# Optimization experiments

Measured on AMD Instinct MI355X. Metric: run time of the kernel, lower is better.

The kernel has to match this reference:

```python
import jax, jax.numpy as jnp
import numpy as np

B, N_TOK, C = 16, 4096, 512
TIME_DIM = 512
H_HEADS, WS = 8, 8
HEAD_DIM = C // H_HEADS
RES = 64  # sqrt(N_TOK)
NH = NW = RES // WS
SCALE = HEAD_DIM ** -0.5


def _rel_pos_index(ws):
    coords = np.stack(np.meshgrid(np.arange(ws), np.arange(ws), indexing='ij'))  # (2,ws,ws)
    flat = coords.reshape(2, -1)  # (2, ws*ws)
    rel = flat[:, :, None] - flat[:, None, :]  # (2, N, N)
    rel = rel.transpose(1, 2, 0).astype(np.int64)
    rel[:, :, 0] += ws - 1
    rel[:, :, 1] += ws - 1
    rel[:, :, 0] *= 2 * ws - 1
    return rel.sum(-1)  # (ws*ws, ws*ws)

REL_IDX = jnp.asarray(_rel_pos_index(WS))


def setup_inputs() -> dict:
    key = jax.random.key(0)
    ks = jax.random.split(key, 9)
    return {
        'x': jax.random.normal(ks[0], (B, N_TOK, C), jnp.float32),
        'time_emb': jax.random.normal(ks[1], (B, TIME_DIM), jnp.float32),
        'Wqkv': jax.random.normal(ks[2], (3 * C, C), jnp.float32) * 0.02,
        'bqkv': jnp.zeros((3 * C,), jnp.float32),
        'Wt': jax.random.normal(ks[3], (3 * C, TIME_DIM), jnp.float32) * 0.02,
        'bt': jnp.zeros((3 * C,), jnp.float32),
        'Wo': jax.random.normal(ks[4], (C, C), jnp.float32) * 0.02,
        'bo': jnp.zeros((C,), jnp.float32),
        'bias_table': jax.random.normal(ks[5], ((2 * WS - 1) ** 2, H_HEADS), jnp.float32) * 0.02,
    }


def reference(x, time_emb, Wqkv, bqkv, Wt, bt, Wo, bo, bias_table):
    Bo = x.shape[0]
    # window partition: (B, H*W, C) -> (B*nH*nW, ws*ws, C)
    xw = x.reshape(Bo, NH, WS, NW, WS, C).transpose(0, 1, 3, 2, 4, 5).reshape(-1, WS * WS, C)
    Bw, N = xw.shape[0], WS * WS
    # time emb broadcast to every window: (Bw, time_dim)
    te = jnp.broadcast_to(time_emb[:, None, :], (Bo, NH * NW, TIME_DIM)).reshape(Bw, TIME_DIM)
    # spatial qkv: (Bw, N, 3, h, d) -> q/k/v (Bw, h, N, d)
    qkv_s = (xw @ Wqkv.T + bqkv).reshape(Bw, N, 3, H_HEADS, HEAD_DIM).transpose(2, 0, 3, 1, 4)
    # time qkv: (Bw, 3, h, d) -> (3, Bw, h, 1, d)
    qkv_t = (te @ Wt.T + bt).reshape(Bw, 1, 3, H_HEADS, HEAD_DIM).transpose(2, 0, 3, 1, 4)
    q = qkv_s[0] + qkv_t[0]
    k = qkv_s[1] + qkv_t[1]
    v = qkv_s[2] + qkv_t[2]
    # relative position bias: (h, N, N)
    bias = bias_table[REL_IDX.reshape(-1)].reshape(N, N, H_HEADS).transpose(2, 0, 1)
    attn = jnp.einsum('bhnd,bhmd->bhnm', q, k) * SCALE + bias[None]
    attn = jax.nn.softmax(attn, axis=-1)
    out = jnp.einsum('bhnm,bhmd->bhnd', attn, v)
    out = out.transpose(0, 2, 1, 3).reshape(Bw, N, C)
    out = out @ Wo.T + bo
    # NOTE: source module's unpartition condition (ws^2 < ws^2) is False -> stays windowed
    return out
```

## Files before the change

### kernel.cpp

```cpp
#include <hip/hip_runtime.h>

using u16 = unsigned short;
typedef __bf16 bf16x8 __attribute__((ext_vector_type(8)));
typedef float floatx4 __attribute__((ext_vector_type(4)));

__device__ __forceinline__ u16 f2bf(float f) {
    union { float f; unsigned u; } v; v.f = f;
    unsigned r = v.u + 0x7fffu + ((v.u >> 16) & 1u);
    return (u16)(r >> 16);
}

__device__ __forceinline__ void gld16(const void* g, void* l) {
    __builtin_amdgcn_global_load_lds(
        (const __attribute__((address_space(1))) void*)g,
        (__attribute__((address_space(3))) void*)l, 16, 0, 0);
}

__device__ __forceinline__ void cvt4(const float* __restrict__ src,
                                     u16* __restrict__ dst, int i) {
    float4 v = *(const float4*)(src + i);
    ushort4 o;
    o.x = f2bf(v.x); o.y = f2bf(v.y); o.z = f2bf(v.z); o.w = f2bf(v.w);
    *(ushort4*)(dst + i) = o;
}

__global__ __launch_bounds__(256) void prep_k(
    const float* __restrict__ x, const float* __restrict__ Wqkv,
    const float* __restrict__ Wo, const float* __restrict__ te,
    const float* __restrict__ Wt, const float* __restrict__ bt,
    const float* __restrict__ btab,
    u16* __restrict__ xbf, u16* __restrict__ wqkvbf, u16* __restrict__ wobf,
    float* __restrict__ qkvt, float* __restrict__ biasf)
{
    const int b = blockIdx.x, tid = threadIdx.x;
    if (b < 768) {
        cvt4(Wqkv, wqkvbf, b * 1024 + tid * 4);
    } else if (b < 1024) {
        cvt4(Wo, wobf, (b - 768) * 1024 + tid * 4);
    } else if (b < 1120) {
        const int bb = b - 1024;
        const int batch = bb / 6;
        const int c = (bb % 6) * 256 + tid;
        const float4* a4 = (const float4*)(te + batch * 512);
        const float4* w4 = (const float4*)(Wt + (size_t)c * 512);
        float s = 0.f;
        for (int i = 0; i < 128; ++i) {
            float4 av = a4[i], wv = w4[i];
            s += av.x * wv.x + av.y * wv.y + av.z * wv.z + av.w * wv.w;
        }
        qkvt[batch * 1536 + c] = s + bt[c];
    } else if (b < 1152) {
        const int e0 = (b - 1120) * 1024 + tid;
        for (int k = 0; k < 4; ++k) {
            int e = e0 + k * 256;
            int h = e >> 12, rc = e & 4095, row = rc >> 6, col = rc & 63;
            int idx = ((row >> 3) - (col >> 3) + 7) * 15 + ((row & 7) - (col & 7) + 7);
            biasf[e] = btab[idx * 8 + h];
        }
    } else {
        const int base = (b - 1152) * 4096 + tid * 4;
        for (int k = 0; k < 4; ++k) cvt4(x, xbf, base + k * 1024);
    }
}

__global__ __launch_bounds__(256, 3) void gemm_qkv_k(
    const u16* __restrict__ A, const u16* __restrict__ B,
    const float* __restrict__ bqkv, const float* __restrict__ qkvt,
    u16* __restrict__ C)
{
    __shared__ __align__(16) u16 lA[128 * 32];
    __shared__ __align__(16) u16 lB[128 * 32];
    const int tid = threadIdx.x;
    const int lane = tid & 63, wv = tid >> 6;
    const int ln = lane & 15, quad = lane >> 4;

    const int orig = blockIdx.y * 12 + blockIdx.x;
    const int wgid = (orig & 7) * 768 + (orig >> 3);
    const int tm = wgid / 12, tn = wgid % 12;

    const int wm = (wv & 1) * 64, wn = (wv >> 1) * 64;

    floatx4 acc[4][4];
#pragma unroll
    for (int i = 0; i < 4; ++i)
#pragma unroll
        for (int j = 0; j < 4; ++j) acc[i][j] = (floatx4){0.f, 0.f, 0.f, 0.f};

    const int srow = tid >> 2, scb = tid & 3;
    const u16* ag = A + (size_t)(tm * 128 + srow) * 512 + scb * 8;
    const u16* bg = B + (size_t)(tn * 128 + srow) * 512 + scb * 8;
    u16* la0 = &lA[tid * 8];
    u16* la1 = &lA[2048 + tid * 8];
    u16* lb0 = &lB[tid * 8];
    u16* lb1 = &lB[2048 + tid * 8];

    for (int k0 = 0; k0 < 512; k0 += 32) {
        __syncthreads();
        gld16(ag + k0, la0);
        gld16(ag + 64 * 512 + k0, la1);
        gld16(bg + k0, lb0);
        gld16(bg + 64 * 512 + k0, lb1);
        __syncthreads();
        bf16x8 af[4], bf[4];
#pragma unroll
        for (int mt = 0; mt < 4; ++mt)
            af[mt] = *(const bf16x8*)&lA[(wm + mt * 16 + ln) * 32 + quad * 8];
#pragma unroll
        for (int nt = 0; nt < 4; ++nt)
            bf[nt] = *(const bf16x8*)&lB[(wn + nt * 16 + ln) * 32 + quad * 8];
#pragma unroll
        for (int mt = 0; mt < 4; ++mt)
#pragma unroll
            for (int nt = 0; nt < 4; ++nt)
                acc[mt][nt] = __builtin_amdgcn_mfma_f32_16x16x32_bf16(
                    af[mt], bf[nt], acc[mt][nt], 0, 0, 0);
    }

    const float* qt = qkvt + (tm >> 5) * 1536;
#pragma unroll
    for (int nt = 0; nt < 4; ++nt) {
        const int col = tn * 128 + wn + nt * 16 + ln;
        const float add = bqkv[col] + qt[col];
#pragma unroll
        for (int mt = 0; mt < 4; ++mt) {
            const int row0 = tm * 128 + wm + mt * 16 + quad * 4;
#pragma unroll
            for (int r = 0; r < 4; ++r)
                C[(size_t)(row0 + r) * 1536 + col] = f2bf(acc[mt][nt][r] + add);
        }
    }
}

__global__ __launch_bounds__(256, 4) void attn_k(
    const u16* __restrict__ qkv, const float* __restrict__ biasf,
    u16* __restrict__ aout)
{
    __shared__ __align__(16) u16 sbuf[4][64 * 72];
    const int tid = threadIdx.x, lane = tid & 63, wv = tid >> 6;
    const int ln = lane & 15, quad = lane >> 4;
    const int pair = blockIdx.x * 4 + wv;
    const int w = pair >> 3, h = pair & 7;
    const int bb = w >> 6, nh = (w >> 3) & 7, nw = w & 7;
    const int tbase = bb * 4096 + nh * 512 + nw * 8;
    u16* buf = sbuf[wv];

    {
        const int wj = lane >> 3;
        const int d0 = (lane & 7) * 8;
#pragma unroll
        for (int i = 0; i < 8; ++i) {
            const int t = tbase + i * 64 + wj;
            union { bf16x8 v; u16 u[8]; } cv;
            cv.v = *(const bf16x8*)(qkv + (size_t)t * 1536 + 1024 + h * 64 + d0);
            const int n = i * 8 + wj;
#pragma unroll
            for (int j = 0; j < 8; ++j) buf[(d0 + j) * 72 + n] = cv.u[j];
        }
    }

    bf16x8 vtf[4][2];
#pragma unroll
    for (int dt = 0; dt < 4; ++dt) {
        const u16* vr = &buf[(dt * 16 + ln) * 72 + quad * 8];
        vtf[dt][0] = *(const bf16x8*)vr;
        vtf[dt][1] = *(const bf16x8*)(vr + 32);
    }

    bf16x8 kf[4][2];
#pragma unroll
    for (int nt = 0; nt < 4; ++nt) {
        const int n = nt * 16 + ln;
        const int t = tbase + (n >> 3) * 64 + (n & 7);
        const u16* kr = qkv + (size_t)t * 1536 + 512 + h * 64 + quad * 8;
        kf[nt][0] = *(const bf16x8*)kr;
        kf[nt][1] = *(const bf16x8*)(kr + 32);
    }

#pragma unroll
    for (int mt = 0; mt < 4; ++mt) {
        const int m = mt * 16 + ln;
        const int t = tbase + (m >> 3) * 64 + (m & 7);
        const u16* qr = qkv + (size_t)t * 1536 + h * 64 + quad * 8;
        const bf16x8 qf0 = *(const bf16x8*)qr;
        const bf16x8 qf1 = *(const bf16x8*)(qr + 32);
        floatx4 s[4];
        __builtin_amdgcn_s_setprio(1);
#pragma unroll
        for (int nt = 0; nt < 4; ++nt) {
            s[nt] = (floatx4){0.f, 0.f, 0.f, 0.f};
            s[nt] = __builtin_amdgcn_mfma_f32_16x16x32_bf16(qf0, kf[nt][0], s[nt], 0, 0, 0);
            s[nt] = __builtin_amdgcn_mfma_f32_16x16x32_bf16(qf1, kf[nt][1], s[nt], 0, 0, 0);
        }
        __builtin_amdgcn_s_setprio(0);
        float z[4][4];
        const float* bptr = biasf + h * 4096 + (mt * 16 + quad * 4) * 64 + ln;
#pragma unroll
        for (int nt = 0; nt < 4; ++nt)
#pragma unroll
            for (int r = 0; r < 4; ++r)
                z[nt][r] = s[nt][r] * 0.125f + bptr[r * 64 + nt * 16];
        float pmax[4], prcp[4];
#pragma unroll
        for (int r = 0; r < 4; ++r) {
            float v = fmaxf(fmaxf(z[0][r], z[1][r]), fmaxf(z[2][r], z[3][r]));
            v = fmaxf(v, __shfl_xor(v, 1));
            v = fmaxf(v, __shfl_xor(v, 2));
            v = fmaxf(v, __shfl_xor(v, 4));
            v = fmaxf(v, __shfl_xor(v, 8));
            pmax[r] = v;
        }
#pragma unroll
        for (int nt = 0; nt < 4; ++nt)
#pragma unroll
            for (int r = 0; r < 4; ++r)
                z[nt][r] = __expf(z[nt][r] - pmax[r]);
#pragma unroll
        for (int r = 0; r < 4; ++r) {
            float v = z[0][r] + z[1][r] + z[2][r] + z[3][r];
            v += __shfl_xor(v, 1);
            v += __shfl_xor(v, 2);
            v += __shfl_xor(v, 4);
            v += __shfl_xor(v, 8);
            prcp[r] = __builtin_amdgcn_rcpf(v);
        }
#pragma unroll
        for (int nt = 0; nt < 4; ++nt)
#pragma unroll
            for (int r = 0; r < 4; ++r)
                buf[(mt * 16 + quad * 4 + r) * 72 + nt * 16 + ln] =
                    f2bf(z[nt][r] * prcp[r]);
    }

#pragma unroll
    for (int mt = 0; mt < 4; ++mt) {
        const u16* pr = &buf[(mt * 16 + ln) * 72 + quad * 8];
        const bf16x8 pf0 = *(const bf16x8*)pr;
        const bf16x8 pf1 = *(const bf16x8*)(pr + 32);
#pragma unroll
        for (int dt = 0; dt < 4; ++dt) {
            floatx4 o = (floatx4){0.f, 0.f, 0.f, 0.f};
            __builtin_amdgcn_s_setprio(1);
            o = __builtin_amdgcn_mfma_f32_16x16x32_bf16(pf0, vtf[dt][0], o, 0, 0, 0);
            o = __builtin_amdgcn_mfma_f32_16x16x32_bf16(pf1, vtf[dt][1], o, 0, 0, 0);
            __builtin_amdgcn_s_setprio(0);
            const size_t rbase =
                (size_t)(w * 64 + mt * 16 + quad * 4) * 512 + h * 64 + dt * 16 + ln;
#pragma unroll
            for (int r = 0; r < 4; ++r)
                aout[rbase + (size_t)r * 512] = f2bf(o[r]);
        }
    }
}

__global__ __launch_bounds__(256, 3) void gemm_out_k(
    const u16* __restrict__ A, const u16* __restrict__ B,
    const float* __restrict__ bo, float* __restrict__ C)
{
    __shared__ __align__(16) u16 lA[128 * 32];
    __shared__ __align__(16) u16 lB[128 * 32];
    const int tid = threadIdx.x;
    const int lane = tid & 63, wv = tid >> 6;
    const int ln = lane & 15, quad = lane >> 4;

    const int orig = blockIdx.y * 4 + blockIdx.x;
    const int wgid = (orig & 7) * 256 + (orig >> 3);
    const int tm = wgid >> 2, tn = wgid & 3;

    const int wm = (wv & 1) * 64, wn = (wv >> 1) * 64;

    floatx4 acc[4][4];
#pragma unroll
    for (int i = 0; i < 4; ++i)
#pragma unroll
        for (int j = 0; j < 4; ++j) acc[i][j] = (floatx4){0.f, 0.f, 0.f, 0.f};

    const int srow = tid >> 2, scb = tid & 3;
    const u16* ag = A + (size_t)(tm * 128 + srow) * 512 + scb * 8;
    const u16* bg = B + (size_t)(tn * 128 + srow) * 512 + scb * 8;
    u16* la0 = &lA[tid * 8];
    u16* la1 = &lA[2048 + tid * 8];
    u16* lb0 = &lB[tid * 8];
    u16* lb1 = &lB[2048 + tid * 8];

    for (int k0 = 0; k0 < 512; k0 += 32) {
        __syncthreads();
        gld16(ag + k0, la0);
        gld16(ag + 64 * 512 + k0, la1);
        gld16(bg + k0, lb0);
        gld16(bg + 64 * 512 + k0, lb1);
        __syncthreads();
        bf16x8 af[4], bf[4];
#pragma unroll
        for (int mt = 0; mt < 4; ++mt)
            af[mt] = *(const bf16x8*)&lA[(wm + mt * 16 + ln) * 32 + quad * 8];
#pragma unroll
        for (int nt = 0; nt < 4; ++nt)
            bf[nt] = *(const bf16x8*)&lB[(wn + nt * 16 + ln) * 32 + quad * 8];
#pragma unroll
        for (int mt = 0; mt < 4; ++mt)
#pragma unroll
            for (int nt = 0; nt < 4; ++nt)
                acc[mt][nt] = __builtin_amdgcn_mfma_f32_16x16x32_bf16(
                    af[mt], bf[nt], acc[mt][nt], 0, 0, 0);
    }

#pragma unroll
    for (int nt = 0; nt < 4; ++nt) {
        const int col = tn * 128 + wn + nt * 16 + ln;
        const float add = bo[col];
#pragma unroll
        for (int mt = 0; mt < 4; ++mt) {
            const int row0 = tm * 128 + wm + mt * 16 + quad * 4;
#pragma unroll
            for (int r = 0; r < 4; ++r)
                C[(size_t)(row0 + r) * 512 + col] = acc[mt][nt][r] + add;
        }
    }
}

extern "C" void kernel_launch(void* const* d_in, const int* in_sizes, int n_in,
                              void* d_out, int out_size, void* d_ws, size_t ws_size,
                              hipStream_t stream)
{
    const float* x    = (const float*)d_in[0];
    const float* te   = (const float*)d_in[1];
    const float* Wqkv = (const float*)d_in[2];
    const float* bqkv = (const float*)d_in[3];
    const float* Wt   = (const float*)d_in[4];
    const float* bt   = (const float*)d_in[5];
    const float* Wo   = (const float*)d_in[6];
    const float* bo   = (const float*)d_in[7];
    const float* btab = (const float*)d_in[8];
    float* out = (float*)d_out;

    char* w = (char*)d_ws;
    u16*   xbf    = (u16*)(w);
    u16*   qkvbf  = (u16*)(w + 67108864);
    u16*   wqkvbf = (u16*)(w + 268435456);
    u16*   wobf   = (u16*)(w + 270008320);
    float* qkvt   = (float*)(w + 270532608);
    float* biasf  = (float*)(w + 270630912);

    prep_k<<<9344, 256, 0, stream>>>(x, Wqkv, Wo, te, Wt, bt, btab,
                                     xbf, wqkvbf, wobf, qkvt, biasf);
    gemm_qkv_k<<<dim3(12, 512), 256, 0, stream>>>(xbf, wqkvbf, bqkv, qkvt, qkvbf);
    attn_k<<<2048, 256, 0, stream>>>(qkvbf, biasf, xbf );
    gemm_out_k<<<dim3(4, 512), 256, 0, stream>>>(xbf, wobf, bo, out);
}
```

Before: 507.1 us.

## Fuse four kernels into one persistent cooperative kernel with grid syncs

```diff
diff --git a/kernel.cpp b/kernel.cpp
--- a/kernel.cpp
+++ b/kernel.cpp
@@ -1,4 +1,7 @@
 #include <hip/hip_runtime.h>
+#include <hip/hip_cooperative_groups.h>
+
+namespace cg = cooperative_groups;
 
 using u16 = unsigned short;
 typedef __bf16 bf16x8 __attribute__((ext_vector_type(8)));
@@ -22,6 +25,311 @@
     ushort4 o;
     o.x = f2bf(v.x); o.y = f2bf(v.y); o.z = f2bf(v.z); o.w = f2bf(v.w);
     *(ushort4*)(dst + i) = o;
+}
+
+__global__ __launch_bounds__(256, 3) void mega_k(
+    const float* __restrict__ x, const float* __restrict__ te,
+    const float* __restrict__ Wqkv, const float* __restrict__ bqkv,
+    const float* __restrict__ Wt, const float* __restrict__ bt,
+    const float* __restrict__ Wo, const float* __restrict__ bo,
+    const float* __restrict__ btab, float* __restrict__ out,
+    char* __restrict__ ws)
+{
+    u16*   xbf    = (u16*)(ws);
+    u16*   qkvbf  = (u16*)(ws + 67108864);
+    u16*   wqkvbf = (u16*)(ws + 268435456);
+    u16*   wobf   = (u16*)(ws + 270008320);
+    float* qkvt   = (float*)(ws + 270532608);
+    float* biasf  = (float*)(ws + 270630912);
+
+    __shared__ __align__(16) u16 smem[18432];
+    u16* lA = smem;
+    u16* lB = smem + 4096;
+
+    cg::grid_group grid = cg::this_grid();
+    const int tid = threadIdx.x;
+    const int lane = tid & 63, wv = tid >> 6;
+    const int ln = lane & 15, quad = lane >> 4;
+    const int nb = gridDim.x;
+
+    for (int b = blockIdx.x; b < 9344; b += nb) {
+        if (b < 768) {
+            cvt4(Wqkv, wqkvbf, b * 1024 + tid * 4);
+        } else if (b < 1024) {
+            cvt4(Wo, wobf, (b - 768) * 1024 + tid * 4);
+        } else if (b < 1120) {
+            const int bb = b - 1024;
+            const int batch = bb / 6;
+            const int c = (bb % 6) * 256 + tid;
+            const float4* a4 = (const float4*)(te + batch * 512);
+            const float4* w4 = (const float4*)(Wt + (size_t)c * 512);
+            float s = 0.f;
+            for (int i = 0; i < 128; ++i) {
+                float4 av = a4[i], wvv = w4[i];
+                s += av.x * wvv.x + av.y * wvv.y + av.z * wvv.z + av.w * wvv.w;
+            }
+            qkvt[batch * 1536 + c] = s + bt[c];
+        } else if (b < 1152) {
+            const int e0 = (b - 1120) * 1024 + tid;
+            for (int k = 0; k < 4; ++k) {
+                int e = e0 + k * 256;
+                int h = e >> 12, rc = e & 4095, row = rc >> 6, col = rc & 63;
+                int idx = ((row >> 3) - (col >> 3) + 7) * 15 + ((row & 7) - (col & 7) + 7);
+                biasf[e] = btab[idx * 8 + h];
+            }
+        } else {
+            const int base = (b - 1152) * 4096 + tid * 4;
+            for (int k = 0; k < 4; ++k) cvt4(x, xbf, base + k * 1024);
+        }
+    }
+
+    __threadfence();
+    grid.sync();
+    __threadfence();
+
+    {
+        const int wm = (wv & 1) * 64, wn = (wv >> 1) * 64;
+        const int srow = tid >> 2, scb = tid & 3;
+        u16* la0 = &lA[tid * 8];
+        u16* la1 = &lA[2048 + tid * 8];
+        u16* lb0 = &lB[tid * 8];
+        u16* lb1 = &lB[2048 + tid * 8];
+
+        for (int v = blockIdx.x; v < 6144; v += nb) {
+            const int wgid = (v & 7) * 768 + (v >> 3);
+            const int tm = wgid / 12, tn = wgid % 12;
+
+            floatx4 acc[4][4];
+#pragma unroll
+            for (int i = 0; i < 4; ++i)
+#pragma unroll
+                for (int j = 0; j < 4; ++j) acc[i][j] = (floatx4){0.f, 0.f, 0.f, 0.f};
+
+            const u16* ag = xbf + (size_t)(tm * 128 + srow) * 512 + scb * 8;
+            const u16* bg = wqkvbf + (size_t)(tn * 128 + srow) * 512 + scb * 8;
+
+            for (int k0 = 0; k0 < 512; k0 += 32) {
+                __syncthreads();
+                gld16(ag + k0, la0);
+                gld16(ag + 64 * 512 + k0, la1);
+                gld16(bg + k0, lb0);
+                gld16(bg + 64 * 512 + k0, lb1);
+                __syncthreads();
+                bf16x8 af[4], bf[4];
+#pragma unroll
+                for (int mt = 0; mt < 4; ++mt)
+                    af[mt] = *(const bf16x8*)&lA[(wm + mt * 16 + ln) * 32 + quad * 8];
+#pragma unroll
+                for (int nt = 0; nt < 4; ++nt)
+                    bf[nt] = *(const bf16x8*)&lB[(wn + nt * 16 + ln) * 32 + quad * 8];
+#pragma unroll
+                for (int mt = 0; mt < 4; ++mt)
+#pragma unroll
+                    for (int nt = 0; nt < 4; ++nt)
+                        acc[mt][nt] = __builtin_amdgcn_mfma_f32_16x16x32_bf16(
+                            af[mt], bf[nt], acc[mt][nt], 0, 0, 0);
+            }
+            __syncthreads();
+
+            const float* qt = qkvt + (tm >> 5) * 1536;
+#pragma unroll
+            for (int nt = 0; nt < 4; ++nt) {
+                const int col = tn * 128 + wn + nt * 16 + ln;
+                const float add = bqkv[col] + qt[col];
+#pragma unroll
+                for (int mt = 0; mt < 4; ++mt) {
+                    const int row0 = tm * 128 + wm + mt * 16 + quad * 4;
+#pragma unroll
+                    for (int r = 0; r < 4; ++r)
+                        qkvbf[(size_t)(row0 + r) * 1536 + col] = f2bf(acc[mt][nt][r] + add);
+                }
+            }
+        }
+    }
+
+    __threadfence();
+    grid.sync();
+    __threadfence();
+
+    {
+        u16* buf = smem + wv * 4608;
+        for (int v = blockIdx.x; v < 2048; v += nb) {
+            const int pair = v * 4 + wv;
+            const int w = pair >> 3, h = pair & 7;
+            const int bb = w >> 6, nh = (w >> 3) & 7, nw = w & 7;
+            const int tbase = bb * 4096 + nh * 512 + nw * 8;
+
+            {
+                const int wj = lane >> 3;
+                const int d0 = (lane & 7) * 8;
+#pragma unroll
+                for (int i = 0; i < 8; ++i) {
+                    const int t = tbase + i * 64 + wj;
+                    union { bf16x8 v; u16 u[8]; } cv;
+                    cv.v = *(const bf16x8*)(qkvbf + (size_t)t * 1536 + 1024 + h * 64 + d0);
+                    const int n = i * 8 + wj;
+#pragma unroll
+                    for (int j = 0; j < 8; ++j) buf[(d0 + j) * 72 + n] = cv.u[j];
+                }
+            }
+
+            bf16x8 vtf[4][2];
+#pragma unroll
+            for (int dt = 0; dt < 4; ++dt) {
+                const u16* vr = &buf[(dt * 16 + ln) * 72 + quad * 8];
+                vtf[dt][0] = *(const bf16x8*)vr;
+                vtf[dt][1] = *(const bf16x8*)(vr + 32);
+            }
+
+            bf16x8 kf[4][2];
+#pragma unroll
+            for (int nt = 0; nt < 4; ++nt) {
+                const int n = nt * 16 + ln;
+                const int t = tbase + (n >> 3) * 64 + (n & 7);
+                const u16* kr = qkvbf + (size_t)t * 1536 + 512 + h * 64 + quad * 8;
+                kf[nt][0] = *(const bf16x8*)kr;
+                kf[nt][1] = *(const bf16x8*)(kr + 32);
+            }
+
+#pragma unroll
+            for (int mt = 0; mt < 4; ++mt) {
+                const int m = mt * 16 + ln;
+                const int t = tbase + (m >> 3) * 64 + (m & 7);
+                const u16* qr = qkvbf + (size_t)t * 1536 + h * 64 + quad * 8;
+                const bf16x8 qf0 = *(const bf16x8*)qr;
+                const bf16x8 qf1 = *(const bf16x8*)(qr + 32);
+                floatx4 s[4];
+                __builtin_amdgcn_s_setprio(1);
+#pragma unroll
+                for (int nt = 0; nt < 4; ++nt) {
+                    s[nt] = (floatx4){0.f, 0.f, 0.f, 0.f};
+                    s[nt] = __builtin_amdgcn_mfma_f32_16x16x32_bf16(qf0, kf[nt][0], s[nt], 0, 0, 0);
+                    s[nt] = __builtin_amdgcn_mfma_f32_16x16x32_bf16(qf1, kf[nt][1], s[nt], 0, 0, 0);
+                }
+                __builtin_amdgcn_s_setprio(0);
+                float z[4][4];
+                const float* bptr = biasf + h * 4096 + (mt * 16 + quad * 4) * 64 + ln;
+#pragma unroll
+                for (int nt = 0; nt < 4; ++nt)
+#pragma unroll
+                    for (int r = 0; r < 4; ++r)
+                        z[nt][r] = s[nt][r] * 0.125f + bptr[r * 64 + nt * 16];
+                float pmax[4], prcp[4];
+#pragma unroll
+                for (int r = 0; r < 4; ++r) {
+                    float vv = fmaxf(fmaxf(z[0][r], z[1][r]), fmaxf(z[2][r], z[3][r]));
+                    vv = fmaxf(vv, __shfl_xor(vv, 1));
+                    vv = fmaxf(vv, __shfl_xor(vv, 2));
+                    vv = fmaxf(vv, __shfl_xor(vv, 4));
+                    vv = fmaxf(vv, __shfl_xor(vv, 8));
+                    pmax[r] = vv;
+                }
+#pragma unroll
+                for (int nt = 0; nt < 4; ++nt)
+#pragma unroll
+                    for (int r = 0; r < 4; ++r)
+                        z[nt][r] = __expf(z[nt][r] - pmax[r]);
+#pragma unroll
+                for (int r = 0; r < 4; ++r) {
+                    float vv = z[0][r] + z[1][r] + z[2][r] + z[3][r];
+                    vv += __shfl_xor(vv, 1);
+                    vv += __shfl_xor(vv, 2);
+                    vv += __shfl_xor(vv, 4);
+                    vv += __shfl_xor(vv, 8);
+                    prcp[r] = __builtin_amdgcn_rcpf(vv);
+                }
+#pragma unroll
+                for (int nt = 0; nt < 4; ++nt)
+#pragma unroll
+                    for (int r = 0; r < 4; ++r)
+                        buf[(mt * 16 + quad * 4 + r) * 72 + nt * 16 + ln] =
+                            f2bf(z[nt][r] * prcp[r]);
+            }
+
+#pragma unroll
+            for (int mt = 0; mt < 4; ++mt) {
+                const u16* pr = &buf[(mt * 16 + ln) * 72 + quad * 8];
+                const bf16x8 pf0 = *(const bf16x8*)pr;
+                const bf16x8 pf1 = *(const bf16x8*)(pr + 32);
+#pragma unroll
+                for (int dt = 0; dt < 4; ++dt) {
+                    floatx4 o = (floatx4){0.f, 0.f, 0.f, 0.f};
+                    __builtin_amdgcn_s_setprio(1);
+                    o = __builtin_amdgcn_mfma_f32_16x16x32_bf16(pf0, vtf[dt][0], o, 0, 0, 0);
+                    o = __builtin_amdgcn_mfma_f32_16x16x32_bf16(pf1, vtf[dt][1], o, 0, 0, 0);
+                    __builtin_amdgcn_s_setprio(0);
+                    const size_t rbase =
+                        (size_t)(w * 64 + mt * 16 + quad * 4) * 512 + h * 64 + dt * 16 + ln;
+#pragma unroll
+                    for (int r = 0; r < 4; ++r)
+                        xbf[rbase + (size_t)r * 512] = f2bf(o[r]);
+                }
+            }
+        }
+    }
+
+    __threadfence();
+    grid.sync();
+    __threadfence();
+
+    {
+        const int wm = (wv & 1) * 64, wn = (wv >> 1) * 64;
+        const int srow = tid >> 2, scb = tid & 3;
+        u16* la0 = &lA[tid * 8];
+        u16* la1 = &lA[2048 + tid * 8];
+        u16* lb0 = &lB[tid * 8];
+        u16* lb1 = &lB[2048 + tid * 8];
+
+        for (int v = blockIdx.x; v < 2048; v += nb) {
+            const int wgid = (v & 7) * 256 + (v >> 3);
+            const int tm = wgid >> 2, tn = wgid & 3;
+
+            floatx4 acc[4][4];
+#pragma unroll
+            for (int i = 0; i < 4; ++i)
+#pragma unroll
+                for (int j = 0; j < 4; ++j) acc[i][j] = (floatx4){0.f, 0.f, 0.f, 0.f};
+
+            const u16* ag = xbf + (size_t)(tm * 128 + srow) * 512 + scb * 8;
+            const u16* bg = wobf + (size_t)(tn * 128 + srow) * 512 + scb * 8;
+
+            for (int k0 = 0; k0 < 512; k0 += 32) {
+                __syncthreads();
+                gld16(ag + k0, la0);
+                gld16(ag + 64 * 512 + k0, la1);
+                gld16(bg + k0, lb0);
+                gld16(bg + 64 * 512 + k0, lb1);
+                __syncthreads();
+                bf16x8 af[4], bf[4];
+#pragma unroll
+                for (int mt = 0; mt < 4; ++mt)
+                    af[mt] = *(const bf16x8*)&lA[(wm + mt * 16 + ln) * 32 + quad * 8];
+#pragma unroll
+                for (int nt = 0; nt < 4; ++nt)
+                    bf[nt] = *(const bf16x8*)&lB[(wn + nt * 16 + ln) * 32 + quad * 8];
+#pragma unroll
+                for (int mt = 0; mt < 4; ++mt)
+#pragma unroll
+                    for (int nt = 0; nt < 4; ++nt)
+                        acc[mt][nt] = __builtin_amdgcn_mfma_f32_16x16x32_bf16(
+                            af[mt], bf[nt], acc[mt][nt], 0, 0, 0);
+            }
+            __syncthreads();
+
+#pragma unroll
+            for (int nt = 0; nt < 4; ++nt) {
+                const int col = tn * 128 + wn + nt * 16 + ln;
+                const float add = bo[col];
+#pragma unroll
+                for (int mt = 0; mt < 4; ++mt) {
+                    const int row0 = tm * 128 + wm + mt * 16 + quad * 4;
+#pragma unroll
+                    for (int r = 0; r < 4; ++r)
+                        out[(size_t)(row0 + r) * 512 + col] = acc[mt][nt][r] + add;
+                }
+            }
+        }
+    }
 }
 
 __global__ __launch_bounds__(256) void prep_k(
@@ -332,18 +640,41 @@
     const float* bo   = (const float*)d_in[7];
     const float* btab = (const float*)d_in[8];
     float* out = (float*)d_out;
-
-    char* w = (char*)d_ws;
-    u16*   xbf    = (u16*)(w);
-    u16*   qkvbf  = (u16*)(w + 67108864);
-    u16*   wqkvbf = (u16*)(w + 268435456);
-    u16*   wobf   = (u16*)(w + 270008320);
-    float* qkvt   = (float*)(w + 270532608);
-    float* biasf  = (float*)(w + 270630912);
+    char* wsp  = (char*)d_ws;
+
+    u16*   xbf    = (u16*)(wsp);
+    u16*   qkvbf  = (u16*)(wsp + 67108864);
+    u16*   wqkvbf = (u16*)(wsp + 268435456);
+    u16*   wobf   = (u16*)(wsp + 270008320);
+    float* qkvt   = (float*)(wsp + 270532608);
+    float* biasf  = (float*)(wsp + 270630912);
+
+    static int coop_grid = -2;
+    if (coop_grid == -2) {
+        int nb = 0;
+        hipError_t e = hipOccupancyMaxActiveBlocksPerMultiprocessor(
+            &nb, mega_k, 256, 0);
+        if (e != hipSuccess || nb < 1) coop_grid = -1;
+        else coop_grid = (nb >= 3) ? 768 : nb * 256;
+        (void)hipGetLastError();
+    }
+
+    if (coop_grid > 0) {
+        void* args[] = {
+            (void*)&x, (void*)&te, (void*)&Wqkv, (void*)&bqkv, (void*)&Wt,
+            (void*)&bt, (void*)&Wo, (void*)&bo, (void*)&btab, (void*)&out,
+            (void*)&wsp
+        };
+        hipError_t le = hipLaunchCooperativeKernel(
+            (const void*)mega_k, dim3(coop_grid), dim3(256), args, 0, stream);
+        if (le == hipSuccess) return;
+        coop_grid = -1;
+        (void)hipGetLastError();
+    }
 
     prep_k<<<9344, 256, 0, stream>>>(x, Wqkv, Wo, te, Wt, bt, btab,
                                      xbf, wqkvbf, wobf, qkvt, biasf);
     gemm_qkv_k<<<dim3(12, 512), 256, 0, stream>>>(xbf, wqkvbf, bqkv, qkvt, qkvbf);
-    attn_k<<<2048, 256, 0, stream>>>(qkvbf, biasf, xbf );
+    attn_k<<<2048, 256, 0, stream>>>(qkvbf, biasf, xbf);
     gemm_out_k<<<dim3(4, 512), 256, 0, stream>>>(xbf, wobf, bo, out);
 }
```

Measured after the change: 898.6 us. 1.77x slower.
